# Optimization experiments

Hardware: AMD Instinct MI355X
Metric: run time of the kernel (lower is better)

## Reference

```python
import jax, jax.numpy as jnp
import numpy as np
from jax import lax

B, L, D_MODEL = 4, 1024, 512
D_STATE, D_CONV, D_INNER = 16, 4, 2 * D_MODEL


def setup_inputs() -> dict:
    key = jax.random.key(0)
    ks = jax.random.split(key, 8)
    s = 0.02
    x = jax.random.normal(ks[0], (B, L, D_MODEL), dtype=jnp.float32)
    W_in = jax.random.normal(ks[1], (D_MODEL, 2 * D_INNER), dtype=jnp.float32) * s
    conv_w = jax.random.normal(ks[2], (D_INNER, 1, D_CONV), dtype=jnp.float32) * s  # OIH, depthwise
    conv_b = jnp.zeros((D_INNER,), jnp.float32)
    W_x = jax.random.normal(ks[3], (D_INNER, 2 * D_STATE), dtype=jnp.float32) * s
    W_dt = jax.random.normal(ks[4], (D_INNER, D_INNER), dtype=jnp.float32) * s
    b_dt = jnp.zeros((D_INNER,), jnp.float32)
    # A_log = -logspace(log10(0.001), log10(1.0), d_state); used directly as A in the scan
    A_log = -jnp.logspace(np.log10(1e-3), 0.0, D_STATE, dtype=jnp.float32)
    D_skip = jnp.ones((D_INNER,), jnp.float32) * 0.1
    W_out = jax.random.normal(ks[5], (D_INNER, D_MODEL), dtype=jnp.float32) * s
    gamma = jnp.ones((D_MODEL,), jnp.float32)
    beta = jnp.zeros((D_MODEL,), jnp.float32)
    return dict(x=x, W_in=W_in, conv_w=conv_w, conv_b=conv_b, W_x=W_x, W_dt=W_dt,
                b_dt=b_dt, A_log=A_log, D_skip=D_skip, W_out=W_out, gamma=gamma, beta=beta)


def _mamba_forward(x, W_in, conv_w, conv_b, W_x, W_dt, b_dt, A_log, D_skip, W_out, gamma, beta):
    x = jnp.clip(x, -10.0, 10.0)
    x_and_res = x @ W_in                                  # [B, L, 2*d_inner]
    xp, res = jnp.split(x_and_res, 2, axis=-1)
    # Depthwise causal conv1d: torch pads d_conv-1 both sides then slices [:L] -> left-pad only.
    xt = jnp.transpose(xp, (0, 2, 1))                     # [B, d_inner, L]
    xc = lax.conv_general_dilated(xt, conv_w, window_strides=(1,),
                                  padding=[(D_CONV - 1, 0)],
                                  dimension_numbers=('NCH', 'OIH', 'NCH'),
                                  feature_group_count=D_INNER)
    xc = xc + conv_b[None, :, None]
    xc = jax.nn.silu(jnp.transpose(xc, (0, 2, 1)))        # [B, L, d_inner]
    ssm = xc @ W_x                                        # [B, L, 2*d_state]
    Bm, Cm = jnp.split(ssm, 2, axis=-1)                   # each [B, L, d_state]
    delta = xc @ W_dt + b_dt                              # [B, L, d_inner] (no softplus in source)

    # Selective scan over time (sequential recurrence)
    def step(h, inp):
        u_t, d_t, B_t, C_t = inp                          # [B,I], [B,I], [B,S], [B,S]
        dA = jnp.exp(jnp.clip(d_t[:, :, None] * A_log, -5.0, 5.0))   # [B, I, S]
        h = dA * h + (d_t[:, :, None] * B_t[:, None, :]) * u_t[:, :, None]
        y = jnp.einsum('bis,bs->bi', h, C_t)
        return h, y

    tm = lambda a: jnp.swapaxes(a, 0, 1)                  # time-major
    h0 = jnp.zeros((x.shape[0], D_INNER, D_STATE), xc.dtype)
    _, ys = lax.scan(step, h0, (tm(xc), tm(delta), tm(Bm), tm(Cm)))
    y = jnp.swapaxes(ys, 0, 1) + xc * D_skip              # D skip connection

    y = y * jax.nn.silu(res)                              # gating
    out = y @ W_out
    r = out + x                                           # residual
    mu = jnp.mean(r, axis=-1, keepdims=True)
    var = jnp.var(r, axis=-1, keepdims=True)
    return gamma * (r - mu) / jnp.sqrt(var + 1e-5) + beta


def reference(x, W_in, conv_w, conv_b, W_x, W_dt, b_dt, A_log, D_skip, W_out, gamma, beta):
    return _mamba_forward(x, W_in, conv_w, conv_b, W_x, W_dt, b_dt, A_log, D_skip, W_out, gamma, beta)
```

## Files before the change

kernel.cpp:

```cpp
#include <hip/hip_runtime.h>
#include <hip/hip_bf16.h>

typedef __hip_bfloat16 bf16;
typedef unsigned short ushort_t;
typedef unsigned int uint_t;
typedef __attribute__((ext_vector_type(8))) __bf16 bf16x8;
typedef __attribute__((ext_vector_type(8))) ushort_t u16x8;
typedef __attribute__((ext_vector_type(4))) ushort_t u16x4;
typedef __attribute__((ext_vector_type(4))) float f32x4;
typedef __attribute__((ext_vector_type(2))) float f32x2;

#define BB 4
#define LL 1024
#define DM 512
#define DS 16
#define DI 1024
#define ROWS 4096
#define NC 64
#define CT 16
#define NDTX 1152
#define LOG2E 1.4426950408889634f

__device__ __forceinline__ float b2f(bf16 v) { return __bfloat162float(v); }

__device__ __forceinline__ float load_flag(const void* src, int i, int isbf)
{
    return isbf ? b2f(((const bf16*)src)[i]) : ((const float*)src)[i];
}

__device__ __forceinline__ ushort_t f2b_bits(float v)
{
    bf16 t = __float2bfloat16(v);
    return *(ushort_t*)&t;
}

__device__ __forceinline__ float bits2f(ushort_t u)
{
    uint_t w = ((uint_t)u) << 16;
    return __uint_as_float(w);
}

__device__ __forceinline__ float exp2fast(float x)
{
#if __has_builtin(__builtin_amdgcn_exp2f)
    return __builtin_amdgcn_exp2f(x);
#else
    float r;
    asm("v_exp_f32 %0, %1" : "=v"(r) : "v"(x));
    return r;
#endif
}

__device__ __forceinline__ int detect_local(const ushort_t* wdt)
{
    __shared__ int bad;
    if (threadIdx.x == 0) bad = 0;
    __syncthreads();
    ushort_t u = wdt[threadIdx.x & 255];
    if (((u >> 7) & 0xFF) >= 127) atomicAdd(&bad, 1);
    __syncthreads();
    return (bad <= 8) ? 1 : 0;
}

__global__ __launch_bounds__(256)
void prep_all(const void* x, const void* Win, const void* Wdt, const void* Wx,
              const void* Wout, const void* cw, const void* cb, const void* Alog,
              const void* Dsk, const void* gam, const void* bet, const void* bdtin,
              bf16* __restrict__ xbf, bf16* __restrict__ WtIn,
              bf16* __restrict__ WtDtx, bf16* __restrict__ WtOut,
              float* __restrict__ ccw, float* __restrict__ ccb,
              float* __restrict__ cAlg, float* __restrict__ cDsk,
              float* __restrict__ cgam, float* __restrict__ cbet,
              float* __restrict__ bdtx)
{
    const int isbf = detect_local((const ushort_t*)Wdt);
    int blk = blockIdx.x;

    if (blk < 2048) {
        int idx = blk * 256 + threadIdx.x;
        float v[4];
        if (isbf) {
            uint2 raw = ((const uint2*)x)[idx];
            v[0] = __uint_as_float(raw.x << 16);
            v[1] = __uint_as_float(raw.x & 0xFFFF0000u);
            v[2] = __uint_as_float(raw.y << 16);
            v[3] = __uint_as_float(raw.y & 0xFFFF0000u);
        } else {
            float4 raw = ((const float4*)x)[idx];
            v[0] = raw.x; v[1] = raw.y; v[2] = raw.z; v[3] = raw.w;
        }
        uint_t b0, b1;
        b0 = f2b_bits(fminf(fmaxf(v[0], -10.f), 10.f))
           | ((uint_t)f2b_bits(fminf(fmaxf(v[1], -10.f), 10.f)) << 16);
        b1 = f2b_bits(fminf(fmaxf(v[2], -10.f), 10.f))
           | ((uint_t)f2b_bits(fminf(fmaxf(v[3], -10.f), 10.f)) << 16);
        uint2 ow; ow.x = b0; ow.y = b1;
        ((uint2*)xbf)[idx] = ow;
    } else if (blk < 4640) {
        int tb = blk - 2048;
        const void* src; bf16* dst; int K, Nsrc, tpr;
        if (tb < 1024)      { src = Win;  dst = WtIn;   K = 512;  Nsrc = 2048; tpr = 64; }
        else if (tb < 2048) { tb -= 1024; src = Wdt;  dst = WtDtx; K = 1024; Nsrc = 1024; tpr = 32; }
        else if (tb < 2080) { tb -= 2048; src = Wx;   dst = WtDtx + 1024 * 1024; K = 1024; Nsrc = 32; tpr = 1; }
        else                { tb -= 2080; src = Wout; dst = WtOut;  K = 1024; Nsrc = 512;  tpr = 16; }
        int k0 = (tb / tpr) * 32, n0 = (tb % tpr) * 32;

        __shared__ float tile[32][33];
        int tx = threadIdx.x & 31, ty = threadIdx.x >> 5;
        #pragma unroll
        for (int j = 0; j < 4; ++j)
            tile[ty + 8 * j][tx] = load_flag(src, (k0 + ty + 8 * j) * Nsrc + n0 + tx, isbf);
        __syncthreads();
        #pragma unroll
        for (int j = 0; j < 4; ++j)
            dst[(size_t)(n0 + ty + 8 * j) * K + k0 + tx] = __float2bfloat16(tile[tx][ty + 8 * j]);
    } else {
        int i = (blk - 4640) * 256 + threadIdx.x;
        if (i < 4096)        ccw[i] = load_flag(cw, i, isbf);
        else if (i < 5120)   ccb[i - 4096] = load_flag(cb, i - 4096, isbf);
        else if (i < 5136)   cAlg[i - 5120] = load_flag(Alog, i - 5120, isbf) * LOG2E;
        else if (i < 6160)   cDsk[i - 5136] = load_flag(Dsk, i - 5136, isbf);
        else if (i < 6672)   cgam[i - 6160] = load_flag(gam, i - 6160, isbf);
        else if (i < 7184)   cbet[i - 6672] = load_flag(bet, i - 6672, isbf);
        else if (i < 8336) {
            int j = i - 7184;
            bdtx[j] = (j < DI) ? load_flag(bdtin, j, isbf) : 0.f;
        } else if (i < 106640) {
            (WtDtx + 1056 * 1024)[i - 8336] = __float2bfloat16(0.f);
        }
    }
}

__device__ __forceinline__ void gload16(const bf16* g, ushort_t* l)
{
    __builtin_amdgcn_global_load_lds(
        (const __attribute__((address_space(1))) void*)g,
        (__attribute__((address_space(3))) void*)l, 16, 0, 0);
}

template <int TM, int TN, bool OBF, bool OT, bool SPLIT>
__global__ __launch_bounds__(256)
void gemm_mfma(const bf16* __restrict__ A, const bf16* __restrict__ Bt,
               const float* __restrict__ bias, void* __restrict__ Cv,
               void* __restrict__ Cv2, int M, int N, int K)
{
    constexpr int MI = TM / 32, NJ = TN / 32;
    constexpr int NQA = TM * 8 / 256;
    constexpr int NQB = TN * 8 / 256;
    __shared__ ushort_t As[TM * 64];
    __shared__ ushort_t Bs[TN * 64];

    const int tid = threadIdx.x;
    const int lane = tid & 63;
    const int w = tid >> 6;
    const int wr = w >> 1, wc = w & 1;

    const int nbx = gridDim.x;
    const int nwg = nbx * gridDim.y;
    int flat = blockIdx.y * nbx + blockIdx.x;
    if ((nwg & 7) == 0) {
        const int cpx = nwg >> 3;
        flat = (flat & 7) * cpx + (flat >> 3);
    }
    const int m0 = (flat / nbx) * TM;
    const int n0 = (flat % nbx) * TN;

    const bf16* gA[NQA]; ushort_t* lA[NQA];
    #pragma unroll
    for (int q = 0; q < NQA; ++q) {
        int p = q * 256 + tid;
        int row = p >> 3, kc = ((p & 7) - row) & 7;
        gA[q] = A + (size_t)(m0 + row) * K + kc * 8;
        lA[q] = &As[(q * 256 + w * 64) * 8];
    }
    const bf16* gB[NQB]; ushort_t* lB[NQB];
    #pragma unroll
    for (int q = 0; q < NQB; ++q) {
        int p = q * 256 + tid;
        int row = p >> 3, kc = ((p & 7) - row) & 7;
        gB[q] = Bt + (size_t)(n0 + row) * K + kc * 8;
        lB[q] = &Bs[(q * 256 + w * 64) * 8];
    }

    f32x4 acc[MI][NJ];
    #pragma unroll
    for (int i = 0; i < MI; ++i)
        #pragma unroll
        for (int j = 0; j < NJ; ++j)
            acc[i][j] = (f32x4){0.f, 0.f, 0.f, 0.f};

    const int ko = lane >> 4;
    const int ml = lane & 15;

    for (int k0 = 0; k0 < K; k0 += 64) {
        #pragma unroll
        for (int q = 0; q < NQA; ++q) gload16(gA[q] + k0, lA[q]);
        #pragma unroll
        for (int q = 0; q < NQB; ++q) gload16(gB[q] + k0, lB[q]);
        __syncthreads();

        #pragma unroll
        for (int half = 0; half < 2; ++half) {
            bf16x8 af[MI], bfr[NJ];
            #pragma unroll
            for (int i = 0; i < MI; ++i) {
                int m = wr * (TM / 2) + i * 16 + ml;
                af[i] = *(const bf16x8*)&As[(m * 8 + ((half * 4 + ko + m) & 7)) * 8];
            }
            #pragma unroll
            for (int j = 0; j < NJ; ++j) {
                int n = wc * (TN / 2) + j * 16 + ml;
                bfr[j] = *(const bf16x8*)&Bs[(n * 8 + ((half * 4 + ko + n) & 7)) * 8];
            }
            #pragma unroll
            for (int i = 0; i < MI; ++i)
                #pragma unroll
                for (int j = 0; j < NJ; ++j)
                    acc[i][j] = __builtin_amdgcn_mfma_f32_16x16x32_bf16(
                        af[i], bfr[j], acc[i][j], 0, 0, 0);
        }
        __syncthreads();
    }

    const int rq = lane >> 4;
    #pragma unroll
    for (int j = 0; j < NJ; ++j) {
        int n = n0 + wc * (TN / 2) + j * 16 + ml;
        float bv = bias ? bias[n] : 0.f;
        #pragma unroll
        for (int i = 0; i < MI; ++i) {
            int mb = m0 + wr * (TM / 2) + i * 16 + rq * 4;
            if (SPLIT && n >= 1024) {
                if (n < 1088) {
                    #pragma unroll
                    for (int r = 0; r < 4; ++r)
                        ((bf16*)Cv2)[(size_t)(mb + r) * 64 + (n - 1024)] =
                            __float2bfloat16(acc[i][j][r] + bv);
                }
            } else if (OT) {
                u16x4 pk;
                #pragma unroll
                for (int r = 0; r < 4; ++r)
                    pk[r] = f2b_bits(acc[i][j][r] + bv);
                *(u16x4*)((ushort_t*)Cv + (size_t)n * M + mb) = pk;
            } else {
                #pragma unroll
                for (int r = 0; r < 4; ++r) {
                    float v = acc[i][j][r] + bv;
                    if (OBF) ((bf16*)Cv)[(size_t)(mb + r) * N + n] = __float2bfloat16(v);
                    else     ((float*)Cv)[(size_t)(mb + r) * N + n] = v;
                }
            }
        }
    }
}

__global__ __launch_bounds__(256)
void conv_silu(const bf16* __restrict__ xrbT, const float* __restrict__ cw,
               const float* __restrict__ cb, bf16* __restrict__ xcT,
               bf16* __restrict__ xc)
{
    __shared__ ushort_t tile[64 * 72];
    const int blk = blockIdx.x;
    const int ch0 = (blk & 15) * 64;
    const int T0b = (blk >> 4) * 64;
    const int lc = threadIdx.x >> 2, tg = threadIdx.x & 3;
    const int i = ch0 + lc;
    const int T0 = T0b + tg * 16;

    const ushort_t* base = (const ushort_t*)xrbT + (size_t)i * ROWS + T0;
    u16x8 m0 = *(const u16x8*)base;
    u16x8 m1 = *(const u16x8*)(base + 8);
    u16x8 pv = {0, 0, 0, 0, 0, 0, 0, 0};
    if ((T0 & (LL - 1)) != 0) pv = *(const u16x8*)(base - 8);

    float4 w = ((const float4*)cw)[i];
    float bs = cb[i];
    float xm3 = bits2f(pv[5]), xm2 = bits2f(pv[6]), xm1 = bits2f(pv[7]);
    u16x8 o0, o1;
    #pragma unroll
    for (int tt = 0; tt < 16; ++tt) {
        float x0 = bits2f(tt < 8 ? m0[tt] : m1[tt - 8]);
        float acc = bs;
        acc = fmaf(xm3, w.x, acc);
        acc = fmaf(xm2, w.y, acc);
        acc = fmaf(xm1, w.z, acc);
        acc = fmaf(x0,  w.w, acc);
        ushort_t ob = f2b_bits(acc / (1.f + __expf(-acc)));
        if (tt < 8) o0[tt] = ob; else o1[tt - 8] = ob;
        xm3 = xm2; xm2 = xm1; xm1 = x0;
    }
    ushort_t* dt = (ushort_t*)xcT + (size_t)i * ROWS + T0;
    *(u16x8*)dt = o0;
    *(u16x8*)(dt + 8) = o1;
    *(u16x8*)&tile[lc * 72 + tg * 16] = o0;
    *(u16x8*)&tile[lc * 72 + tg * 16 + 8] = o1;
    __syncthreads();
    const int lt = threadIdx.x >> 2, cg = threadIdx.x & 3;
    u16x8 q0, q1;
    #pragma unroll
    for (int j = 0; j < 8; ++j) q0[j] = tile[(cg * 16 + j) * 72 + lt];
    #pragma unroll
    for (int j = 8; j < 16; ++j) q1[j - 8] = tile[(cg * 16 + j) * 72 + lt];
    ushort_t* wp = (ushort_t*)xc + (size_t)(T0b + lt) * DI + ch0 + cg * 16;
    *(u16x8*)wp = q0;
    *(u16x8*)(wp + 8) = q1;
}

__global__ __launch_bounds__(1024, 4)
void scan_fused(const bf16* __restrict__ xcT, const bf16* __restrict__ dT,
                const bf16* __restrict__ ssm, const bf16* __restrict__ xrbT,
                const float* __restrict__ A_l2e, const float* __restrict__ Dskip,
                bf16* __restrict__ ybf)
{
    __shared__ uint_t lsum[DS * 1024];

    const int tid = threadIdx.x;
    const int b = blockIdx.x >> 6;
    const int ch0 = (blockIdx.x & 63) << 4;
    const int chl = tid & 15;
    const int c = tid >> 4;
    const int i = ch0 + chl;
    const size_t tb = (size_t)b * LL + c * CT;

    float a[DS];
    #pragma unroll
    for (int s = 0; s < DS; ++s) {
        uint_t bits = (uint_t)__builtin_amdgcn_readfirstlane((int)__float_as_uint(A_l2e[s]));
        a[s] = __uint_as_float(bits);
    }

    const u16x8* dp = (const u16x8*)((const ushort_t*)dT + (size_t)i * ROWS + tb);
    const u16x8* up = (const u16x8*)((const ushort_t*)xcT + (size_t)i * ROWS + tb);
    const u16x8* rp = (const u16x8*)((const ushort_t*)xrbT + (size_t)(1024 + i) * ROWS + tb);
    const ushort_t* sbase = (const ushort_t*)ssm + tb * 64;

    f32x2 h2[8];
    #pragma unroll
    for (int k = 0; k < 8; ++k) h2[k] = (f32x2){0.f, 0.f};
    float cd = 0.f;

    {
        u16x8 dvlo = dp[0], dvhi = dp[1];
        u16x8 uvlo = up[0], uvhi = up[1];
        u16x8 c0a = *(const u16x8*)(sbase);
        u16x8 c0b = *(const u16x8*)(sbase + 8);
        u16x8 c1a = *(const u16x8*)(sbase + 64);
        u16x8 c1b = *(const u16x8*)(sbase + 72);
        #pragma unroll
        for (int tt = 0; tt < 16; ++tt) {
            u16x8 B0 = c0a, B1 = c0b;
            c0a = c1a; c0b = c1b;
            if (tt < 14) {
                c1a = *(const u16x8*)(sbase + (tt + 2) * 64);
                c1b = *(const u16x8*)(sbase + (tt + 2) * 64 + 8);
            }
            float dv = bits2f(tt < 8 ? dvlo[tt] : dvhi[tt - 8]);
            float uv = bits2f(tt < 8 ? uvlo[tt] : uvhi[tt - 8]);
            float du = dv * uv;
            cd += dv;
            f32x2 du2 = {du, du};
            f32x2 dv2 = {dv, dv};
            #pragma unroll
            for (int k = 0; k < 8; ++k) {
                f32x2 av = {a[2 * k], a[2 * k + 1]};
                f32x2 e2 = dv2 * av;
                f32x2 dA = {exp2fast(e2[0]), exp2fast(e2[1])};
                f32x2 Bv = {bits2f(k < 4 ? B0[2 * k] : B1[2 * k - 8]),
                            bits2f(k < 4 ? B0[2 * k + 1] : B1[2 * k - 7])};
                h2[k] = dA * h2[k] + du2 * Bv;
            }
        }
    }

    f32x2 cdf = {cd, cd};
    #pragma unroll
    for (int k = 0; k < 8; ++k) {
        int s0 = 2 * k, s1 = 2 * k + 1;
        f32x2 av = {a[s0], a[s1]};
        f32x2 e2 = cdf * av;
        f32x2 pc = {exp2fast(e2[0]), exp2fast(e2[1])};
        lsum[s0 * 1024 + (tid ^ ((s0 & 1) << 4))] =
            (uint_t)f2b_bits(pc[0]) | ((uint_t)f2b_bits(h2[k][0]) << 16);
        lsum[s1 * 1024 + (tid ^ ((s1 & 1) << 4))] =
            (uint_t)f2b_bits(pc[1]) | ((uint_t)f2b_bits(h2[k][1]) << 16);
    }
    __syncthreads();

    if (tid < 256) {
        int cl = tid & 15, s = tid >> 4;
        int sx = (s & 1) << 4;
        float hh = 0.f;
        for (int cc = 0; cc < NC; ++cc) {
            int off = s * 1024 + ((cc * 16 + cl) ^ sx);
            uint_t wrd = lsum[off];
            float pp = bits2f((ushort_t)(wrd & 0xFFFF));
            float qq = bits2f((ushort_t)(wrd >> 16));
            lsum[off] = (uint_t)f2b_bits(hh);
            hh = fmaf(pp, hh, qq);
        }
    }
    __syncthreads();

    #pragma unroll
    for (int k = 0; k < 8; ++k) {
        int s0 = 2 * k, s1 = 2 * k + 1;
        h2[k][0] = bits2f((ushort_t)lsum[s0 * 1024 + (tid ^ ((s0 & 1) << 4))]);
        h2[k][1] = bits2f((ushort_t)lsum[s1 * 1024 + (tid ^ ((s1 & 1) << 4))]);
    }

    const float dsk = Dskip[i];

    {
        u16x8 dvlo = dp[0], dvhi = dp[1];
        u16x8 uvlo = up[0], uvhi = up[1];
        u16x8 rvlo = rp[0], rvhi = rp[1];
        u16x8 q0a = *(const u16x8*)(sbase);
        u16x8 q0b = *(const u16x8*)(sbase + 8);
        u16x8 q0c = *(const u16x8*)(sbase + 16);
        u16x8 q0d = *(const u16x8*)(sbase + 24);
        #pragma unroll
        for (int tt = 0; tt < 16; ++tt) {
            u16x8 q1a, q1b, q1c, q1d;
            if (tt < 15) {
                q1a = *(const u16x8*)(sbase + (tt + 1) * 64);
                q1b = *(const u16x8*)(sbase + (tt + 1) * 64 + 8);
                q1c = *(const u16x8*)(sbase + (tt + 1) * 64 + 16);
                q1d = *(const u16x8*)(sbase + (tt + 1) * 64 + 24);
            }
            u16x8 B0 = q0a, B1 = q0b, C0 = q0c, C1 = q0d;
            float dv = bits2f(tt < 8 ? dvlo[tt] : dvhi[tt - 8]);
            float uv = bits2f(tt < 8 ? uvlo[tt] : uvhi[tt - 8]);
            float rs = bits2f(tt < 8 ? rvlo[tt] : rvhi[tt - 8]);
            float du = dv * uv;
            f32x2 du2 = {du, du};
            f32x2 dv2 = {dv, dv};
            f32x2 y2 = {0.f, 0.f};
            #pragma unroll
            for (int k = 0; k < 8; ++k) {
                f32x2 av = {a[2 * k], a[2 * k + 1]};
                f32x2 e2 = dv2 * av;
                f32x2 dA = {exp2fast(e2[0]), exp2fast(e2[1])};
                f32x2 Bv = {bits2f(k < 4 ? B0[2 * k] : B1[2 * k - 8]),
                            bits2f(k < 4 ? B0[2 * k + 1] : B1[2 * k - 7])};
                f32x2 Cv = {bits2f(k < 4 ? C0[2 * k] : C1[2 * k - 8]),
                            bits2f(k < 4 ? C0[2 * k + 1] : C1[2 * k - 7])};
                h2[k] = dA * h2[k] + du2 * Bv;
                y2 = y2 + h2[k] * Cv;
            }
            float y = y2[0] + y2[1];
            float g = rs / (1.f + __expf(-rs));
            ybf[(tb + tt) * DI + i] = __float2bfloat16((y + uv * dsk) * g);
            q0a = q1a; q0b = q1b; q0c = q1c; q0d = q1d;
        }
    }
}

__global__ __launch_bounds__(256)
void ln_kernel(const bf16* __restrict__ outp, const void* __restrict__ xsrc,
               const void* __restrict__ wdt_probe,
               const float* __restrict__ gamma, const float* __restrict__ beta,
               void* __restrict__ out)
{
    const int isbf = detect_local((const ushort_t*)wdt_probe);
    const int row = blockIdx.x;
    const int tid = threadIdx.x;

    float r[2];
    float sum = 0.f, ss = 0.f;
    #pragma unroll
    for (int q = 0; q < 2; ++q) {
        int j = tid + q * 256;
        float xv = load_flag(xsrc, row * DM + j, isbf);
        xv = fminf(fmaxf(xv, -10.f), 10.f);
        float v = b2f(outp[(size_t)row * DM + j]) + xv;
        r[q] = v;
        sum += v;
        ss = fmaf(v, v, ss);
    }
    #pragma unroll
    for (int off = 32; off >= 1; off >>= 1) {
        sum += __shfl_down(sum, off);
        ss  += __shfl_down(ss, off);
    }
    __shared__ float s1[4], s2[4];
    __shared__ float stats[2];
    int wid = tid >> 6, lane = tid & 63;
    if (lane == 0) { s1[wid] = sum; s2[wid] = ss; }
    __syncthreads();
    if (tid == 0) {
        float S = s1[0] + s1[1] + s1[2] + s1[3];
        float Qq = s2[0] + s2[1] + s2[2] + s2[3];
        float mean = S / DM;
        float var = Qq / DM - mean * mean;
        stats[0] = mean;
        stats[1] = rsqrtf(var + 1e-5f);
    }
    __syncthreads();
    float mean = stats[0], rstd = stats[1];
    #pragma unroll
    for (int q = 0; q < 2; ++q) {
        int j = tid + q * 256;
        float v = (r[q] - mean) * rstd * gamma[j] + beta[j];
        size_t o = (size_t)row * DM + j;
        if (isbf) ((bf16*)out)[o] = __float2bfloat16(v);
        else      ((float*)out)[o] = v;
    }
}

extern "C" void kernel_launch(void* const* d_in, const int* in_sizes, int n_in,
                              void* d_out, int out_size, void* d_ws, size_t ws_size,
                              hipStream_t stream)
{
    float* W = (float*)d_ws;
    float* ccw  = W;
    float* ccb  = ccw  + 4096;
    float* cAlg = ccb  + 1024;
    float* cDsk = cAlg + 16;
    float* cgam = cDsk + 1024;
    float* cbet = cgam + 512;
    float* bdtx = cbet + 512;
    bf16*  xbf  = (bf16*)(bdtx + 1152);
    bf16*  xrbT = xbf  + 2097152;
    bf16*  xcT  = xrbT + 8388608;
    bf16*  xc   = xcT  + 4194304;
    bf16*  ybf  = xc   + 4194304;
    bf16*  dT   = ybf  + 4194304;
    bf16*  ssm  = dT   + 4194304;
    bf16*  outp = ssm  + 262144;
    bf16*  WtIn = outp + 2097152;
    bf16*  WtDtx= WtIn + 1048576;
    bf16*  WtOut= WtDtx+ 1179648;

    prep_all<<<5057, 256, 0, stream>>>(
        d_in[0], d_in[1], d_in[5], d_in[4], d_in[9], d_in[2], d_in[3],
        d_in[7], d_in[8], d_in[10], d_in[11], d_in[6],
        xbf, WtIn, WtDtx, WtOut, ccw, ccb, cAlg, cDsk, cgam, cbet, bdtx);

    gemm_mfma<128, 128, true, true, false><<<dim3(2048 / 128, ROWS / 128), 256, 0, stream>>>(
        xbf, WtIn, nullptr, xrbT, nullptr, ROWS, 2048, 512);

    conv_silu<<<1024, 256, 0, stream>>>(xrbT, ccw, ccb, xcT, xc);

    gemm_mfma<64, 128, true, true, true><<<dim3(NDTX / 128, ROWS / 64), 256, 0, stream>>>(
        xc, WtDtx, bdtx, dT, ssm, ROWS, NDTX, DI);

    scan_fused<<<256, 1024, 0, stream>>>(xcT, dT, ssm, xrbT, cAlg, cDsk, ybf);

    gemm_mfma<64, 64, true, false, false><<<dim3(DM / 64, ROWS / 64), 256, 0, stream>>>(
        ybf, WtOut, nullptr, outp, nullptr, ROWS, DM, DI);

    ln_kernel<<<ROWS, 256, 0, stream>>>(outp, d_in[0], d_in[5], cgam, cbet, d_out);
}
```

Baseline: 190.6 us.

## Store SSM B/C projections in fp32 and restructure scan loads and carry loop

The split GEMM epilogue now writes the B/C state projections as fp32 instead of bf16, and the scan reads them as float4 vectors. This removes the per-element bf16-to-float conversions in the inner recurrence. In the second pass, C is loaded on demand and the y reduction is split into two accumulators to shorten the dependency chain. The chunk carry loop is unrolled into batched LDS loads and stores. The cost is twice the memory traffic and register footprint for the SSM buffer, plus a new workspace region.

```diff
diff --git a/kernel.cpp b/kernel.cpp
--- a/kernel.cpp
+++ b/kernel.cpp
@@ -234,8 +234,8 @@
                 if (n < 1088) {
                     #pragma unroll
                     for (int r = 0; r < 4; ++r)
-                        ((bf16*)Cv2)[(size_t)(mb + r) * 64 + (n - 1024)] =
-                            __float2bfloat16(acc[i][j][r] + bv);
+                        ((float*)Cv2)[(size_t)(mb + r) * 64 + (n - 1024)] =
+                            acc[i][j][r] + bv;
                 }
             } else if (OT) {
                 u16x4 pk;
@@ -309,7 +309,7 @@
 
 __global__ __launch_bounds__(1024, 4)
 void scan_fused(const bf16* __restrict__ xcT, const bf16* __restrict__ dT,
-                const bf16* __restrict__ ssm, const bf16* __restrict__ xrbT,
+                const float* __restrict__ ssmf, const bf16* __restrict__ xrbT,
                 const float* __restrict__ A_l2e, const float* __restrict__ Dskip,
                 bf16* __restrict__ ybf)
 {
@@ -333,7 +333,7 @@
     const u16x8* dp = (const u16x8*)((const ushort_t*)dT + (size_t)i * ROWS + tb);
     const u16x8* up = (const u16x8*)((const ushort_t*)xcT + (size_t)i * ROWS + tb);
     const u16x8* rp = (const u16x8*)((const ushort_t*)xrbT + (size_t)(1024 + i) * ROWS + tb);
-    const ushort_t* sbase = (const ushort_t*)ssm + tb * 64;
+    const float* sbase = ssmf + tb * 64;
 
     f32x2 h2[8];
     #pragma unroll
@@ -343,17 +343,20 @@
     {
         u16x8 dvlo = dp[0], dvhi = dp[1];
         u16x8 uvlo = up[0], uvhi = up[1];
-        u16x8 c0a = *(const u16x8*)(sbase);
-        u16x8 c0b = *(const u16x8*)(sbase + 8);
-        u16x8 c1a = *(const u16x8*)(sbase + 64);
-        u16x8 c1b = *(const u16x8*)(sbase + 72);
+        f32x4 rB[4], mB[4];
+        #pragma unroll
+        for (int j = 0; j < 4; ++j) rB[j] = *(const f32x4*)(sbase + j * 4);
+        #pragma unroll
+        for (int j = 0; j < 4; ++j) mB[j] = *(const f32x4*)(sbase + 64 + j * 4);
         #pragma unroll
         for (int tt = 0; tt < 16; ++tt) {
-            u16x8 B0 = c0a, B1 = c0b;
-            c0a = c1a; c0b = c1b;
+            f32x4 B[4];
+            #pragma unroll
+            for (int j = 0; j < 4; ++j) { B[j] = rB[j]; rB[j] = mB[j]; }
             if (tt < 14) {
-                c1a = *(const u16x8*)(sbase + (tt + 2) * 64);
-                c1b = *(const u16x8*)(sbase + (tt + 2) * 64 + 8);
+                #pragma unroll
+                for (int j = 0; j < 4; ++j)
+                    mB[j] = *(const f32x4*)(sbase + (tt + 2) * 64 + j * 4);
             }
             float dv = bits2f(tt < 8 ? dvlo[tt] : dvhi[tt - 8]);
             float uv = bits2f(tt < 8 ? uvlo[tt] : uvhi[tt - 8]);
@@ -366,8 +369,7 @@
                 f32x2 av = {a[2 * k], a[2 * k + 1]};
                 f32x2 e2 = dv2 * av;
                 f32x2 dA = {exp2fast(e2[0]), exp2fast(e2[1])};
-                f32x2 Bv = {bits2f(k < 4 ? B0[2 * k] : B1[2 * k - 8]),
-                            bits2f(k < 4 ? B0[2 * k + 1] : B1[2 * k - 7])};
+                f32x2 Bv = {B[k >> 1][(k & 1) * 2], B[k >> 1][(k & 1) * 2 + 1]};
                 h2[k] = dA * h2[k] + du2 * Bv;
             }
         }
@@ -391,13 +393,23 @@
         int cl = tid & 15, s = tid >> 4;
         int sx = (s & 1) << 4;
         float hh = 0.f;
-        for (int cc = 0; cc < NC; ++cc) {
-            int off = s * 1024 + ((cc * 16 + cl) ^ sx);
-            uint_t wrd = lsum[off];
-            float pp = bits2f((ushort_t)(wrd & 0xFFFF));
-            float qq = bits2f((ushort_t)(wrd >> 16));
-            lsum[off] = (uint_t)f2b_bits(hh);
-            hh = fmaf(pp, hh, qq);
+        #pragma unroll
+        for (int cb = 0; cb < 4; ++cb) {
+            uint_t wv[16];
+            #pragma unroll
+            for (int j = 0; j < 16; ++j)
+                wv[j] = lsum[s * 1024 + ((((cb * 16 + j) * 16) + cl) ^ sx)];
+            uint_t hs[16];
+            #pragma unroll
+            for (int j = 0; j < 16; ++j) {
+                hs[j] = (uint_t)f2b_bits(hh);
+                float pp = bits2f((ushort_t)(wv[j] & 0xFFFF));
+                float qq = bits2f((ushort_t)(wv[j] >> 16));
+                hh = fmaf(pp, hh, qq);
+            }
+            #pragma unroll
+            for (int j = 0; j < 16; ++j)
+                lsum[s * 1024 + ((((cb * 16 + j) * 16) + cl) ^ sx)] = hs[j];
         }
     }
     __syncthreads();
@@ -415,43 +427,48 @@
         u16x8 dvlo = dp[0], dvhi = dp[1];
         u16x8 uvlo = up[0], uvhi = up[1];
         u16x8 rvlo = rp[0], rvhi = rp[1];
-        u16x8 q0a = *(const u16x8*)(sbase);
-        u16x8 q0b = *(const u16x8*)(sbase + 8);
-        u16x8 q0c = *(const u16x8*)(sbase + 16);
-        u16x8 q0d = *(const u16x8*)(sbase + 24);
+        f32x4 rB[4], nB[4];
+        #pragma unroll
+        for (int j = 0; j < 4; ++j) rB[j] = *(const f32x4*)(sbase + j * 4);
         #pragma unroll
         for (int tt = 0; tt < 16; ++tt) {
-            u16x8 q1a, q1b, q1c, q1d;
+            f32x4 C[4];
+            #pragma unroll
+            for (int j = 0; j < 4; ++j)
+                C[j] = *(const f32x4*)(sbase + tt * 64 + 16 + j * 4);
             if (tt < 15) {
-                q1a = *(const u16x8*)(sbase + (tt + 1) * 64);
-                q1b = *(const u16x8*)(sbase + (tt + 1) * 64 + 8);
-                q1c = *(const u16x8*)(sbase + (tt + 1) * 64 + 16);
-                q1d = *(const u16x8*)(sbase + (tt + 1) * 64 + 24);
-            }
-            u16x8 B0 = q0a, B1 = q0b, C0 = q0c, C1 = q0d;
+                #pragma unroll
+                for (int j = 0; j < 4; ++j)
+                    nB[j] = *(const f32x4*)(sbase + (tt + 1) * 64 + j * 4);
+            }
             float dv = bits2f(tt < 8 ? dvlo[tt] : dvhi[tt - 8]);
             float uv = bits2f(tt < 8 ? uvlo[tt] : uvhi[tt - 8]);
             float rs = bits2f(tt < 8 ? rvlo[tt] : rvhi[tt - 8]);
             float du = dv * uv;
             f32x2 du2 = {du, du};
             f32x2 dv2 = {dv, dv};
-            f32x2 y2 = {0.f, 0.f};
             #pragma unroll
             for (int k = 0; k < 8; ++k) {
                 f32x2 av = {a[2 * k], a[2 * k + 1]};
                 f32x2 e2 = dv2 * av;
                 f32x2 dA = {exp2fast(e2[0]), exp2fast(e2[1])};
-                f32x2 Bv = {bits2f(k < 4 ? B0[2 * k] : B1[2 * k - 8]),
-                            bits2f(k < 4 ? B0[2 * k + 1] : B1[2 * k - 7])};
-                f32x2 Cv = {bits2f(k < 4 ? C0[2 * k] : C1[2 * k - 8]),
-                            bits2f(k < 4 ? C0[2 * k + 1] : C1[2 * k - 7])};
+                f32x2 Bv = {rB[k >> 1][(k & 1) * 2], rB[k >> 1][(k & 1) * 2 + 1]};
                 h2[k] = dA * h2[k] + du2 * Bv;
-                y2 = y2 + h2[k] * Cv;
-            }
+            }
+            f32x2 y2a = {0.f, 0.f}, y2b = {0.f, 0.f};
+            #pragma unroll
+            for (int k = 0; k < 8; k += 2) {
+                f32x2 Cva = {C[k >> 1][0], C[k >> 1][1]};
+                f32x2 Cvb = {C[k >> 1][2], C[k >> 1][3]};
+                y2a = y2a + h2[k] * Cva;
+                y2b = y2b + h2[k + 1] * Cvb;
+            }
+            f32x2 y2 = y2a + y2b;
             float y = y2[0] + y2[1];
             float g = rs / (1.f + __expf(-rs));
             ybf[(tb + tt) * DI + i] = __float2bfloat16((y + uv * dsk) * g);
-            q0a = q1a; q0b = q1b; q0c = q1c; q0d = q1d;
+            #pragma unroll
+            for (int j = 0; j < 4; ++j) rB[j] = nB[j];
         }
     }
 }
@@ -526,11 +543,12 @@
     bf16*  xc   = xcT  + 4194304;
     bf16*  ybf  = xc   + 4194304;
     bf16*  dT   = ybf  + 4194304;
-    bf16*  ssm  = dT   + 4194304;
-    bf16*  outp = ssm  + 262144;
+    bf16*  ssm0 = dT   + 4194304;
+    bf16*  outp = ssm0 + 262144;
     bf16*  WtIn = outp + 2097152;
     bf16*  WtDtx= WtIn + 1048576;
     bf16*  WtOut= WtDtx+ 1179648;
+    float* ssmf = (float*)(WtOut + 524288);
 
     prep_all<<<5057, 256, 0, stream>>>(
         d_in[0], d_in[1], d_in[5], d_in[4], d_in[9], d_in[2], d_in[3],
@@ -543,9 +561,9 @@
     conv_silu<<<1024, 256, 0, stream>>>(xrbT, ccw, ccb, xcT, xc);
 
     gemm_mfma<64, 128, true, true, true><<<dim3(NDTX / 128, ROWS / 64), 256, 0, stream>>>(
-        xc, WtDtx, bdtx, dT, ssm, ROWS, NDTX, DI);
-
-    scan_fused<<<256, 1024, 0, stream>>>(xcT, dT, ssm, xrbT, cAlg, cDsk, ybf);
+        xc, WtDtx, bdtx, dT, ssmf, ROWS, NDTX, DI);
+
+    scan_fused<<<256, 1024, 0, stream>>>(xcT, dT, ssmf, xrbT, cAlg, cDsk, ybf);
 
     gemm_mfma<64, 64, true, false, false><<<dim3(DM / 64, ROWS / 64), 256, 0, stream>>>(
         ybf, WtOut, nullptr, outp, nullptr, ROWS, DM, DI);
```

Measured after the change: 190.6 us, median of 2. About the same (-0.0%).
